# Performance work log

Measured on AMD Instinct MI355X. Metric: run time of the kernel, lower is better.

The kernel has to match this reference:

```python
import jax, jax.numpy as jnp
import numpy as np

CUT = 512          # cut_size
H = W = 4096       # sideY, sideX (square -> reflect pad in original is a no-op)
N_INNER = 12       # cut_innercut[999-300]
CUT_POW = 1.0
GRAY_W = (0.2989, 0.587, 0.114)  # torchvision rgb_to_grayscale weights


def _gray(x):
    # x: [..., 3, h, w] -> replicate luma over 3 channels (T.Grayscale(3))
    w = jnp.asarray(GRAY_W, x.dtype)
    g = jnp.einsum('...chw,c->...hw', x, w)
    return jnp.broadcast_to(g[..., None, :, :], x.shape)


def _crop_resize(img, offy, offx, size):
    # Bilinear resize of img[:, offy:offy+size, offx:offx+size] to [3, CUT, CUT].
    # Implements crop+resize as a fused bilinear gather (align_corners=False mapping).
    s = size.astype(jnp.float32)
    t = (jnp.arange(CUT, dtype=jnp.float32) + 0.5) * s / CUT - 0.5
    y = jnp.clip(offy + t, offy, offy + s - 1.0)
    x = jnp.clip(offx + t, offx, offx + s - 1.0)
    y0 = jnp.floor(y).astype(jnp.int32)
    x0 = jnp.floor(x).astype(jnp.int32)
    y1 = jnp.minimum(y0 + 1, offy + size - 1)
    x1 = jnp.minimum(x0 + 1, offx + size - 1)
    wy = (y - y0)[None, :, None]
    wx = (x - x0)[None, None, :]
    g = lambda yy, xx: img[:, yy][:, :, xx]  # [3, CUT, CUT]
    top = g(y0, x0) * (1.0 - wx) + g(y0, x1) * wx
    bot = g(y1, x0) * (1.0 - wx) + g(y1, x1) * wx
    return top * (1.0 - wy) + bot * wy


def setup_inputs() -> dict:
    key = jax.random.key(0)
    k1, k2, k3, k4 = jax.random.split(key, 4)
    inp = jax.random.uniform(k1, (1, 3, H, W), jnp.float32)
    min_size = min(H, W, CUT)
    max_size = min(H, W)
    u = jax.random.uniform(k2, (N_INNER,))
    sizes = (u ** CUT_POW * (max_size - min_size) + min_size).astype(jnp.int32)
    offy = (jax.random.uniform(k3, (N_INNER,)) * (H - sizes + 1)).astype(jnp.int32)
    offx = (jax.random.uniform(k4, (N_INNER,)) * (W - sizes + 1)).astype(jnp.int32)
    return {"input": inp, "t": 300, "sizes": sizes, "offy": offy, "offx": offx}


def reference(input, t, sizes, offy, offx):
    # t=300 -> overview=4, inner_crop=12, ic_grey_p=0 (counts baked into static shapes)
    img = input[0]  # [3, H, W]; reflect pad is a no-op for a square image
    full = _crop_resize(img, jnp.int32(0), jnp.int32(0), jnp.int32(min(H, W)))
    flipped = full[..., ::-1]
    overview = jnp.stack([full, _gray(full), flipped, _gray(flipped)])  # [4,3,CUT,CUT]
    inner = jax.vmap(lambda oy, ox, s: _crop_resize(img, oy, ox, s))(offy, offx, sizes)
    # i <= int(0 * 12) -> only inner crop 0 is grayscaled
    inner = inner.at[0].set(_gray(inner[0]))
    return jnp.concatenate([overview, inner], axis=0)  # [16, 3, CUT, CUT]
```

## Files before the change

### kernel.cpp

```cpp
#include <hip/hip_runtime.h>

#define CUT 512
#define HH 4096
#define WW 4096

__device__ __forceinline__ void coord(int i, int off, int size, float s,
                                      int& c0, int& c1, float& w) {
    float t = ((i + 0.5f) * s) / 512.0f - 0.5f;
    float offf = (float)off;
    float v = off + t;
    v = fminf(fmaxf(v, offf), offf + s - 1.0f);
    c0 = (int)floorf(v);
    c1 = min(c0 + 1, off + size - 1);
    w = v - (float)c0;
}

__device__ __forceinline__ float bilerp(const float* __restrict__ p,
                                        int y0, int y1, int x0, int x1,
                                        float wy, float wx) {
    float a  = p[(size_t)y0 * WW + x0];
    float b  = p[(size_t)y0 * WW + x1];
    float c  = p[(size_t)y1 * WW + x0];
    float d  = p[(size_t)y1 * WW + x1];
    float top = a * (1.0f - wx) + b * wx;
    float bot = c * (1.0f - wx) + d * wx;
    return top * (1.0f - wy) + bot * wy;
}

__global__ void overview_kernel(const float* __restrict__ img,
                                float* __restrict__ out) {
    int j = blockIdx.x * blockDim.x + threadIdx.x;
    int i = blockIdx.y;
    if (j >= CUT) return;

    const int size = 4096;
    const float s = 4096.0f;
    int y0, y1, x0, x1;
    float wy, wx;
    coord(i, 0, size, s, y0, y1, wy);
    coord(j, 0, size, s, x0, x1, wx);

    float v[3];
#pragma unroll
    for (int c = 0; c < 3; ++c) {
        const float* p = img + (size_t)c * HH * WW;
        v[c] = bilerp(p, y0, y1, x0, x1, wy, wx);
    }
    float gray = v[0] * 0.2989f + v[1] * 0.587f + v[2] * 0.114f;

    const size_t imgStride = (size_t)3 * CUT * CUT;
    const size_t chStride  = (size_t)CUT * CUT;
    size_t px  = (size_t)i * CUT + j;
    size_t pxf = (size_t)i * CUT + (CUT - 1 - j);

#pragma unroll
    for (int c = 0; c < 3; ++c) {
        out[0 * imgStride + c * chStride + px]  = v[c];
        out[1 * imgStride + c * chStride + px]  = gray;
        out[2 * imgStride + c * chStride + pxf] = v[c];
        out[3 * imgStride + c * chStride + pxf] = gray;
    }
}

__global__ void inner_kernel(const float* __restrict__ img,
                             const int* __restrict__ sizes,
                             const int* __restrict__ offy,
                             const int* __restrict__ offx,
                             float* __restrict__ out) {
    int k = blockIdx.z;
    int j = blockIdx.x * blockDim.x + threadIdx.x;
    int i = blockIdx.y;
    if (j >= CUT) return;

    int size = sizes[k];
    int oy = offy[k];
    int ox = offx[k];
    float s = (float)size;

    int y0, y1, x0, x1;
    float wy, wx;
    coord(i, oy, size, s, y0, y1, wy);
    coord(j, ox, size, s, x0, x1, wx);

    float v[3];
#pragma unroll
    for (int c = 0; c < 3; ++c) {
        const float* p = img + (size_t)c * HH * WW;
        v[c] = bilerp(p, y0, y1, x0, x1, wy, wx);
    }

    const size_t imgStride = (size_t)3 * CUT * CUT;
    const size_t chStride  = (size_t)CUT * CUT;
    size_t base = (size_t)(4 + k) * imgStride;
    size_t px = (size_t)i * CUT + j;

    if (k == 0) {
        float gray = v[0] * 0.2989f + v[1] * 0.587f + v[2] * 0.114f;
#pragma unroll
        for (int c = 0; c < 3; ++c)
            out[base + c * chStride + px] = gray;
    } else {
#pragma unroll
        for (int c = 0; c < 3; ++c)
            out[base + c * chStride + px] = v[c];
    }
}

extern "C" void kernel_launch(void* const* d_in, const int* in_sizes, int n_in,
                              void* d_out, int out_size, void* d_ws, size_t ws_size,
                              hipStream_t stream) {
    const float* img  = (const float*)d_in[0];
    const int* sizes  = (const int*)d_in[2];
    const int* offy   = (const int*)d_in[3];
    const int* offx   = (const int*)d_in[4];
    float* out = (float*)d_out;

    dim3 block(256, 1, 1);
    dim3 gridOv((CUT + 255) / 256, CUT, 1);
    hipLaunchKernelGGL(overview_kernel, gridOv, block, 0, stream, img, out);

    dim3 gridIn((CUT + 255) / 256, CUT, 12);
    hipLaunchKernelGGL(inner_kernel, gridIn, block, 0, stream,
                       img, sizes, offy, offx, out);
}
```

Measured before the change: 299.7 us.

## Fuse overview and inner crops into one kernel with LDS-staged source rows

Merges the overview and inner-crop kernels into a single launch that indexes the image by blockIdx.z. Each block loads the two source rows it needs (all three channels) into shared memory with contiguous, coalesced reads over the x span its 256 outputs cover. It then does the bilinear taps from LDS through an XOR swizzle meant to reduce bank conflicts. The goal is to replace scattered strided global gathers with coalesced row loads. In exchange it adds 48KB of LDS per block, which limits occupancy, and for large downscales it reads whole contiguous spans (up to 2048 wide) even where the taps are sparse.

```diff
diff --git a/kernel.cpp b/kernel.cpp
--- a/kernel.cpp
+++ b/kernel.cpp
@@ -3,6 +3,10 @@
 #define CUT 512
 #define HH 4096
 #define WW 4096
+#define SPAN 2048
+#define NIMG 13
+
+__device__ __forceinline__ int sw(int x) { return x ^ ((x >> 5) & 31); }
 
 __device__ __forceinline__ void coord(int i, int off, int size, float s,
                                       int& c0, int& c1, float& w) {
@@ -15,94 +19,95 @@
     w = v - (float)c0;
 }
 
-__device__ __forceinline__ float bilerp(const float* __restrict__ p,
-                                        int y0, int y1, int x0, int x1,
-                                        float wy, float wx) {
-    float a  = p[(size_t)y0 * WW + x0];
-    float b  = p[(size_t)y0 * WW + x1];
-    float c  = p[(size_t)y1 * WW + x0];
-    float d  = p[(size_t)y1 * WW + x1];
-    float top = a * (1.0f - wx) + b * wx;
-    float bot = c * (1.0f - wx) + d * wx;
-    return top * (1.0f - wy) + bot * wy;
-}
+__global__ __launch_bounds__(256)
+void cutouts_kernel(const float* __restrict__ img,
+                    const int* __restrict__ sizes,
+                    const int* __restrict__ offy,
+                    const int* __restrict__ offx,
+                    float* __restrict__ out) {
+    __shared__ float rows[3][2][SPAN];
 
-__global__ void overview_kernel(const float* __restrict__ img,
-                                float* __restrict__ out) {
-    int j = blockIdx.x * blockDim.x + threadIdx.x;
-    int i = blockIdx.y;
-    if (j >= CUT) return;
+    const int z   = blockIdx.z;
+    const int i   = blockIdx.y;
+    const int jt  = blockIdx.x * 256;
+    const int tid = threadIdx.x;
+    const int j   = jt + tid;
 
-    const int size = 4096;
-    const float s = 4096.0f;
-    int y0, y1, x0, x1;
-    float wy, wx;
-    coord(i, 0, size, s, y0, y1, wy);
-    coord(j, 0, size, s, x0, x1, wx);
+    int size, oy, ox;
+    if (z == 0) { size = 4096; oy = 0; ox = 0; }
+    else        { size = sizes[z - 1]; oy = offy[z - 1]; ox = offx[z - 1]; }
+    const float s = (float)size;
+
+    int y0, y1; float wy;
+    coord(i, oy, size, s, y0, y1, wy);
+
+    int xlo, xhi, dmy; float wd;
+    coord(jt,       ox, size, s, xlo, dmy, wd);
+    coord(jt + 255, ox, size, s, dmy, xhi, wd);
+    const int span = xhi - xlo + 1;
+
+    const float* r00 = img + (size_t)0 * HH * WW + (size_t)y0 * WW + xlo;
+    const float* r01 = img + (size_t)0 * HH * WW + (size_t)y1 * WW + xlo;
+    const float* r10 = img + (size_t)1 * HH * WW + (size_t)y0 * WW + xlo;
+    const float* r11 = img + (size_t)1 * HH * WW + (size_t)y1 * WW + xlo;
+    const float* r20 = img + (size_t)2 * HH * WW + (size_t)y0 * WW + xlo;
+    const float* r21 = img + (size_t)2 * HH * WW + (size_t)y1 * WW + xlo;
+
+    for (int idx = tid; idx < span; idx += 256) {
+        int si = sw(idx);
+        rows[0][0][si] = r00[idx];
+        rows[0][1][si] = r01[idx];
+        rows[1][0][si] = r10[idx];
+        rows[1][1][si] = r11[idx];
+        rows[2][0][si] = r20[idx];
+        rows[2][1][si] = r21[idx];
+    }
+    __syncthreads();
+
+    int x0, x1; float wx;
+    coord(j, ox, size, s, x0, x1, wx);
+    const int l0 = sw(x0 - xlo);
+    const int l1 = sw(x1 - xlo);
 
     float v[3];
 #pragma unroll
     for (int c = 0; c < 3; ++c) {
-        const float* p = img + (size_t)c * HH * WW;
-        v[c] = bilerp(p, y0, y1, x0, x1, wy, wx);
-    }
-    float gray = v[0] * 0.2989f + v[1] * 0.587f + v[2] * 0.114f;
-
-    const size_t imgStride = (size_t)3 * CUT * CUT;
-    const size_t chStride  = (size_t)CUT * CUT;
-    size_t px  = (size_t)i * CUT + j;
-    size_t pxf = (size_t)i * CUT + (CUT - 1 - j);
-
-#pragma unroll
-    for (int c = 0; c < 3; ++c) {
-        out[0 * imgStride + c * chStride + px]  = v[c];
-        out[1 * imgStride + c * chStride + px]  = gray;
-        out[2 * imgStride + c * chStride + pxf] = v[c];
-        out[3 * imgStride + c * chStride + pxf] = gray;
-    }
-}
-
-__global__ void inner_kernel(const float* __restrict__ img,
-                             const int* __restrict__ sizes,
-                             const int* __restrict__ offy,
-                             const int* __restrict__ offx,
-                             float* __restrict__ out) {
-    int k = blockIdx.z;
-    int j = blockIdx.x * blockDim.x + threadIdx.x;
-    int i = blockIdx.y;
-    if (j >= CUT) return;
-
-    int size = sizes[k];
-    int oy = offy[k];
-    int ox = offx[k];
-    float s = (float)size;
-
-    int y0, y1, x0, x1;
-    float wy, wx;
-    coord(i, oy, size, s, y0, y1, wy);
-    coord(j, ox, size, s, x0, x1, wx);
-
-    float v[3];
-#pragma unroll
-    for (int c = 0; c < 3; ++c) {
-        const float* p = img + (size_t)c * HH * WW;
-        v[c] = bilerp(p, y0, y1, x0, x1, wy, wx);
+        float a = rows[c][0][l0];
+        float b = rows[c][0][l1];
+        float cc = rows[c][1][l0];
+        float d = rows[c][1][l1];
+        float top = a * (1.0f - wx) + b * wx;
+        float bot = cc * (1.0f - wx) + d * wx;
+        v[c] = top * (1.0f - wy) + bot * wy;
     }
 
     const size_t imgStride = (size_t)3 * CUT * CUT;
     const size_t chStride  = (size_t)CUT * CUT;
-    size_t base = (size_t)(4 + k) * imgStride;
-    size_t px = (size_t)i * CUT + j;
+    const size_t px  = (size_t)i * CUT + j;
 
-    if (k == 0) {
+    if (z == 0) {
         float gray = v[0] * 0.2989f + v[1] * 0.587f + v[2] * 0.114f;
+        const size_t pxf = (size_t)i * CUT + (CUT - 1 - j);
 #pragma unroll
-        for (int c = 0; c < 3; ++c)
-            out[base + c * chStride + px] = gray;
+        for (int c = 0; c < 3; ++c) {
+            out[0 * imgStride + c * chStride + px]  = v[c];
+            out[1 * imgStride + c * chStride + px]  = gray;
+            out[2 * imgStride + c * chStride + pxf] = v[c];
+            out[3 * imgStride + c * chStride + pxf] = gray;
+        }
     } else {
+        const int k = z - 1;
+        const size_t base = (size_t)(4 + k) * imgStride;
+        if (k == 0) {
+            float gray = v[0] * 0.2989f + v[1] * 0.587f + v[2] * 0.114f;
 #pragma unroll
-        for (int c = 0; c < 3; ++c)
-            out[base + c * chStride + px] = v[c];
+            for (int c = 0; c < 3; ++c)
+                out[base + c * chStride + px] = gray;
+        } else {
+#pragma unroll
+            for (int c = 0; c < 3; ++c)
+                out[base + c * chStride + px] = v[c];
+        }
     }
 }
 
@@ -116,10 +121,7 @@
     float* out = (float*)d_out;
 
     dim3 block(256, 1, 1);
-    dim3 gridOv((CUT + 255) / 256, CUT, 1);
-    hipLaunchKernelGGL(overview_kernel, gridOv, block, 0, stream, img, out);
-
-    dim3 gridIn((CUT + 255) / 256, CUT, 12);
-    hipLaunchKernelGGL(inner_kernel, gridIn, block, 0, stream,
+    dim3 grid(CUT / 256, CUT, NIMG);
+    hipLaunchKernelGGL(cutouts_kernel, grid, block, 0, stream,
                        img, sizes, offy, offx, out);
 }
```

Result: slower. 312.2 us (+4.2%).
